# Performance work log

Measured on AMD Instinct MI355X. Metric: run time of the kernel, lower is better.

The kernel has to match this reference:

```python
import jax, jax.numpy as jnp
import numpy as np

EMBED_DIM = 1024
Q_HEADS = 8
KV_HEADS = 4
HEAD_DIM = EMBED_DIM // Q_HEADS          # 128
KV_EMBED_DIM = HEAD_DIM * KV_HEADS       # 512
LN_EPS = 1e-5
RMS_EPS = 1e-6


def _activation_quant(x):
    # per-token int8 quant over last dim
    scale = 127.0 / jnp.clip(jnp.max(jnp.abs(x), axis=-1, keepdims=True), 1e-5)
    return jnp.clip(jnp.round(x * scale), -128, 127) / scale


def _weight_quant(w):
    # ternary (sign) quant with global mean-abs scale
    scale = jnp.mean(jnp.abs(w))
    e = jnp.mean(w)
    return jnp.sign(w - e) * scale


def bit_linear(x, w):
    # fresh RMSNorm with weight=ones (as in the torch code: RMSNorm(d)(x))
    x_norm = x * jax.lax.rsqrt(jnp.mean(x * x, axis=-1, keepdims=True) + RMS_EPS)
    # straight-through estimators
    x_q = x_norm + jax.lax.stop_gradient(_activation_quant(x_norm) - x_norm)
    w_q = w + jax.lax.stop_gradient(_weight_quant(w) - w)
    # F.linear(x_quant, w_quant): NO bias (the torch forward ignores self.bias)
    return jnp.einsum('bnd,od->bno', x_q, w_q)


def setup_inputs() -> dict:
    key = jax.random.key(0)
    ks = jax.random.split(key, 7)
    B, S = 4, 2048

    def xavier(k, shape):
        std = (2.0 / (shape[0] + shape[1])) ** 0.5
        return std * jax.random.normal(k, shape, dtype=jnp.float32)

    return {
        'query': jax.random.normal(ks[0], (B, S, EMBED_DIM), dtype=jnp.float32),
        'key':   jax.random.normal(ks[1], (B, S, EMBED_DIM), dtype=jnp.float32),
        'value': jax.random.normal(ks[2], (B, S, EMBED_DIM), dtype=jnp.float32),
        'q_w':   xavier(ks[3], (EMBED_DIM, EMBED_DIM)),
        'k_w':   xavier(ks[4], (KV_EMBED_DIM, EMBED_DIM)),
        'v_w':   xavier(ks[5], (KV_EMBED_DIM, EMBED_DIM)),
        'out_w': xavier(ks[6], (EMBED_DIM, KV_EMBED_DIM)),
        'ln_gamma': jnp.ones((KV_EMBED_DIM,), dtype=jnp.float32),
        'ln_beta':  jnp.zeros((KV_EMBED_DIM,), dtype=jnp.float32),
    }


def reference(query, key, value, q_w, k_w, v_w, out_w, ln_gamma, ln_beta):
    B, N, _ = query.shape
    q = bit_linear(query, q_w)   # [b, n, embed_dim]
    k = bit_linear(key,   k_w)   # [b, s, kv_embed_dim]
    v = bit_linear(value, v_w)   # [b, s, kv_embed_dim]

    g = Q_HEADS // KV_HEADS  # head groups
    # b n (hq d) -> b hq n d -> b hk g n d  (head index = h*g + g_idx, matching
    # einops 'b (h g) n d -> b g h n d')
    q = q.reshape(B, N, Q_HEADS, HEAD_DIM).transpose(0, 2, 1, 3)
    q = q.reshape(B, KV_HEADS, g, N, HEAD_DIM)
    k = k.reshape(B, -1, KV_HEADS, HEAD_DIM).transpose(0, 2, 1, 3)  # b h s d
    v = v.reshape(B, -1, KV_HEADS, HEAD_DIM).transpose(0, 2, 1, 3)  # b h s d

    scale = HEAD_DIM ** 0.5
    q = q / scale
    # note: the original SUMS over the group axis g (faithful to einops einsum)
    sim = jnp.einsum('bhgnd,bhsd->bhns', q, k)
    # note: original divides by scale AGAIN before softmax
    attn = jax.nn.softmax(sim / scale, axis=-1)
    out = jnp.einsum('bhns,bhsd->bnhd', attn, v)        # b n hk d
    x = out.reshape(B, N, KV_EMBED_DIM)

    # LayerNorm over kv_embed_dim
    mu = jnp.mean(x, axis=-1, keepdims=True)
    var = jnp.mean((x - mu) ** 2, axis=-1, keepdims=True)
    x = (x - mu) * jax.lax.rsqrt(var + LN_EPS) * ln_gamma + ln_beta

    return bit_linear(x, out_w)  # [b, n, embed_dim]
```

## Files before the change

kernel.cpp:

```cpp
#include <hip/hip_runtime.h>
#include <cstdint>
#include <cstddef>

constexpr int B_   = 4;
constexpr int SEQ  = 2048;
constexpr int E    = 1024;
constexpr int KVE  = 512;
constexpr int H    = 4;
constexpr int ROWS = B_ * SEQ;
constexpr int NSPLIT = 2;
constexpr int KVT  = SEQ / NSPLIT;
constexpr int NT   = KVT / 64;

typedef short short8   __attribute__((ext_vector_type(8)));
typedef short short4v  __attribute__((ext_vector_type(4)));
typedef float floatx4  __attribute__((ext_vector_type(4)));
typedef float floatx16 __attribute__((ext_vector_type(16)));
typedef int   intx4    __attribute__((ext_vector_type(4)));

__device__ inline short f2bf(float f) {
    uint32_t u = __builtin_bit_cast(uint32_t, f);
    u = (u + 0x7fff + ((u >> 16) & 1)) >> 16;
    return (short)u;
}
__device__ inline float bf2f(short s) {
    return __builtin_bit_cast(float, (uint32_t)(uint16_t)s << 16);
}
__device__ inline void gl_lds16(const void* g, void* l) {
    __builtin_amdgcn_global_load_lds(
        (const __attribute__((address_space(1))) unsigned int*)g,
        (__attribute__((address_space(3))) unsigned int*)l, 16, 0, 0);
}

__global__ __launch_bounds__(256) void pre_kernel(
    const float* __restrict__ qx, const float* __restrict__ kx,
    const float* __restrict__ vx,
    const float* __restrict__ w0, const float* __restrict__ w1,
    const float* __restrict__ w2, const float* __restrict__ w3,
    int8_t* __restrict__ xq01, int8_t* __restrict__ xq2,
    float* __restrict__ dqv, float* __restrict__ stats)
{
    int tid = threadIdx.x, bid = blockIdx.x;
    int lane = tid & 63, wv = tid >> 6;
    if (bid < 256) {
        int m = bid >> 6;
        const float* w = (m == 0) ? w0 : (m == 1) ? w1 : (m == 2) ? w2 : w3;
        int n4 = ((m == 0) ? 1024 * 1024 : 512 * 1024) >> 2;
        float s = 0.f, sa = 0.f;
        for (int i = (bid & 63) * 256 + tid; i < n4; i += 64 * 256) {
            float4 x = ((const float4*)w)[i];
            s += x.x + x.y + x.z + x.w;
            sa += fabsf(x.x) + fabsf(x.y) + fabsf(x.z) + fabsf(x.w);
        }
#pragma unroll
        for (int o = 32; o; o >>= 1) { s += __shfl_xor(s, o); sa += __shfl_xor(sa, o); }
        __shared__ float ls[4], lsa[4];
        if (!lane) { ls[wv] = s; lsa[wv] = sa; }
        __syncthreads();
        if (!tid) {
            atomicAdd(&stats[2 * m],     ls[0] + ls[1] + ls[2] + ls[3]);
            atomicAdd(&stats[2 * m + 1], lsa[0] + lsa[1] + lsa[2] + lsa[3]);
        }
        return;
    }
    int rowi = (bid - 256) * 4 + wv;
    int z = rowi >> 13, r = rowi & (ROWS - 1);
    const float* x = (z == 0) ? qx : (z == 1) ? kx : vx;
    int8_t* xq = (z == 2) ? xq2 : xq01 + (size_t)z * ROWS * E;
    size_t base = (size_t)r * E;
    float4 v[4];
    float ss = 0.f, am = 0.f;
#pragma unroll
    for (int j = 0; j < 4; j++) {
        v[j] = *(const float4*)(x + base + lane * 4 + j * 256);
        ss += v[j].x * v[j].x + v[j].y * v[j].y + v[j].z * v[j].z + v[j].w * v[j].w;
        am = fmaxf(am, fmaxf(fmaxf(fabsf(v[j].x), fabsf(v[j].y)),
                             fmaxf(fabsf(v[j].z), fabsf(v[j].w))));
    }
#pragma unroll
    for (int o = 32; o; o >>= 1) { ss += __shfl_xor(ss, o); am = fmaxf(am, __shfl_xor(am, o)); }
    float rms = rsqrtf(ss * (1.0f / E) + 1e-6f);
    float cl  = fmaxf(am * rms, 1e-5f);
    float kf  = rms * (127.0f / cl);
#pragma unroll
    for (int j = 0; j < 4; j++) {
        int q0 = max(-128, min(127, (int)rintf(v[j].x * kf)));
        int q1 = max(-128, min(127, (int)rintf(v[j].y * kf)));
        int q2 = max(-128, min(127, (int)rintf(v[j].z * kf)));
        int q3 = max(-128, min(127, (int)rintf(v[j].w * kf)));
        uint32_t pk = (uint32_t)(q0 & 0xff) | ((uint32_t)(q1 & 0xff) << 8) |
                      ((uint32_t)(q2 & 0xff) << 16) | ((uint32_t)(q3 & 0xff) << 24);
        *(uint32_t*)(xq + base + lane * 4 + j * 256) = pk;
    }
    if (!lane) dqv[(size_t)z * ROWS + r] = cl * (1.0f / 127.0f);
}

__global__ __launch_bounds__(256) void wquant_kernel(
    const float* __restrict__ w0, const float* __restrict__ w1,
    const float* __restrict__ w2, const float* __restrict__ w3,
    int n0, int n1, int n2, int n3, const float* __restrict__ stats,
    int8_t* __restrict__ o0, int8_t* __restrict__ o1,
    int8_t* __restrict__ o2, int8_t* __restrict__ o3)
{
    int m = blockIdx.y;
    const float* w = (m == 0) ? w0 : (m == 1) ? w1 : (m == 2) ? w2 : w3;
    int n = (m == 0) ? n0 : (m == 1) ? n1 : (m == 2) ? n2 : n3;
    int8_t* o = (m == 0) ? o0 : (m == 1) ? o1 : (m == 2) ? o2 : o3;
    float e = stats[2 * m] / (float)n;
    int n4 = n >> 2;
    for (int i = blockIdx.x * 256 + threadIdx.x; i < n4; i += gridDim.x * 256) {
        float4 x = ((const float4*)w)[i];
        int q0 = (x.x > e) - (x.x < e);
        int q1 = (x.y > e) - (x.y < e);
        int q2 = (x.z > e) - (x.z < e);
        int q3 = (x.w > e) - (x.w < e);
        uint32_t pk = (uint32_t)(q0 & 0xff) | ((uint32_t)(q1 & 0xff) << 8) |
                      ((uint32_t)(q2 & 0xff) << 16) | ((uint32_t)(q3 & 0xff) << 24);
        *(uint32_t*)(o + ((size_t)i << 2)) = pk;
    }
}

template <bool F32OUT>
__device__ inline void gemm_body(
    const int8_t* __restrict__ A, const int8_t* __restrict__ W,
    const float* __restrict__ dqv, float sw, void* __restrict__ Cout,
    int O, int K, int8_t* As, int8_t* Ws, size_t row0, size_t c0)
{
    int tid = threadIdx.x;
    int w = tid >> 6, lane = tid & 63;
    int quad = lane >> 4, l15 = lane & 15;
    int mbase = (w & 1) * 64, nbase = (w >> 1) * 64;

    intx4 acc[4][4];
#pragma unroll
    for (int i = 0; i < 4; i++)
#pragma unroll
        for (int j = 0; j < 4; j++) acc[i][j] = (intx4){0, 0, 0, 0};

    const int8_t* Ag[4]; const int8_t* Wg[4]; int8_t* lA[4]; int8_t* lW[4];
#pragma unroll
    for (int t = 0; t < 4; t++) {
        int c = tid + t * 256;
        int row = c >> 3, g = (c & 7) ^ (row & 7);
        Ag[t] = A + (row0 + row) * K + g * 16;
        Wg[t] = W + (c0 + row) * K + g * 16;
        lA[t] = As + c * 16;
        lW[t] = Ws + c * 16;
    }

    for (int kt = 0; kt < K; kt += 128) {
        __syncthreads();
#pragma unroll
        for (int t = 0; t < 4; t++) {
            gl_lds16(Ag[t] + kt, lA[t]);
            gl_lds16(Wg[t] + kt, lW[t]);
        }
        __syncthreads();
#pragma unroll
        for (int kh = 0; kh < 2; kh++) {
            intx4 af[4], bfr[4];
#pragma unroll
            for (int mt = 0; mt < 4; mt++) {
                int row = mbase + mt * 16 + l15;
                int pos = (quad + 4 * kh) ^ (row & 7);
                af[mt] = *(const intx4*)(As + row * 128 + pos * 16);
            }
#pragma unroll
            for (int nt = 0; nt < 4; nt++) {
                int row = nbase + nt * 16 + l15;
                int pos = (quad + 4 * kh) ^ (row & 7);
                bfr[nt] = *(const intx4*)(Ws + row * 128 + pos * 16);
            }
#pragma unroll
            for (int mt = 0; mt < 4; mt++)
#pragma unroll
                for (int nt = 0; nt < 4; nt++)
                    acc[mt][nt] = __builtin_amdgcn_mfma_i32_16x16x64_i8(
                        af[mt], bfr[nt], acc[mt][nt], 0, 0, 0);
        }
    }

#pragma unroll
    for (int mt = 0; mt < 4; mt++) {
#pragma unroll
        for (int r = 0; r < 4; r++) {
            size_t grow = row0 + mbase + mt * 16 + quad * 4 + r;
            float scv = sw * dqv[grow];
#pragma unroll
            for (int nt = 0; nt < 4; nt++) {
                size_t gcol = c0 + nbase + nt * 16 + l15;
                float v = (float)acc[mt][nt][r] * scv;
                if constexpr (F32OUT) ((float*)Cout)[grow * O + gcol] = v;
                else                  ((short*)Cout)[grow * O + gcol] = f2bf(v);
            }
        }
    }
}

__global__ __launch_bounds__(256) void gemm_qkv(
    const int8_t* __restrict__ xq01, const int8_t* __restrict__ xq2,
    const int8_t* __restrict__ wq_q, const int8_t* __restrict__ wq_k,
    const int8_t* __restrict__ wq_v, const float* __restrict__ dqv,
    const float* __restrict__ stats,
    short* __restrict__ qb, short* __restrict__ kb, short* __restrict__ vb)
{
    __shared__ int8_t As[128 * 128];
    __shared__ int8_t Ws[128 * 128];
    int id = blockIdx.x;
    int z, bx, by;
    if (id < 512)      { z = 0; bx = id & 7; by = id >> 3; }
    else if (id < 768) { z = 1; int t = id - 512; bx = t & 3; by = t >> 2; }
    else               { z = 2; int t = id - 768; bx = t & 3; by = t >> 2; }
    int O = z ? KVE : E;
    const int8_t* A = (z == 0) ? xq01 : (z == 1) ? xq01 + (size_t)ROWS * E : xq2;
    const int8_t* W = (z == 0) ? wq_q : (z == 1) ? wq_k : wq_v;
    short* outp = (z == 0) ? qb : (z == 1) ? kb : vb;
    float sw = stats[2 * z + 1] / (float)(O * E);
    gemm_body<false>(A, W, dqv + (size_t)z * ROWS, sw, outp, O, E, As, Ws,
                     (size_t)by * 128, (size_t)bx * 128);
}

__global__ __launch_bounds__(256) void gemm_out(
    const int8_t* __restrict__ A, const int8_t* __restrict__ W,
    const float* __restrict__ dqv, const float* __restrict__ stats,
    float* __restrict__ Cout)
{
    __shared__ int8_t As[128 * 128];
    __shared__ int8_t Ws[128 * 128];
    float sw = stats[7] / (float)(E * KVE);
    gemm_body<true>(A, W, dqv, sw, Cout, E, KVE, As, Ws,
                    (size_t)blockIdx.y * 128, (size_t)blockIdx.x * 128);
}

__global__ __launch_bounds__(256, 2) void attn_mfma(
    const short* __restrict__ qb, const short* __restrict__ kb,
    const short* __restrict__ vb, short* __restrict__ opart,
    float* __restrict__ mlbuf)
{
    __shared__ short Ks[64][132];
    __shared__ short Vt[128][68];
    int tid = threadIdx.x;
    int w = tid >> 6, lane = tid & 63;
    int l31 = lane & 31, hi = lane >> 5;
    int blk = blockIdx.x, h = blockIdx.y, part = blockIdx.z;
    int b = blk >> 4;
    size_t qrow0 = (size_t)blk * 128;
    size_t sbase = (size_t)b * SEQ + (size_t)part * KVT;

    int sK = tid >> 2, cK = tid & 3;
    int sV = (tid & 15) * 4, dV = tid >> 4;

    short8 kreg[4], vreg[4];
    {
        const short* ksrc = kb + (sbase + sK) * KVE + h * 128 + cK * 32;
#pragma unroll
        for (int j = 0; j < 4; j++) kreg[j] = *(const short8*)(ksrc + j * 8);
        const short* vsrc = vb + (sbase + sV) * KVE + h * 128 + dV * 8;
#pragma unroll
        for (int j = 0; j < 4; j++) vreg[j] = *(const short8*)(vsrc + j * KVE);
    }

    short8 qfrag[8];
    {
        const short* src = qb + (qrow0 + w * 32 + l31) * E + h * 256 + hi * 8;
        constexpr float C = 1.44269504089f * (1.0f / 128.0f);
#pragma unroll
        for (int j = 0; j < 8; j++) {
            short8 a  = *(const short8*)(src + j * 16);
            short8 b2 = *(const short8*)(src + j * 16 + 128);
            short8 o;
#pragma unroll
            for (int e = 0; e < 8; e++)
                o[e] = f2bf((bf2f(a[e]) + bf2f(b2[e])) * C);
            qfrag[j] = o;
        }
    }

    floatx16 oacc[4];
#pragma unroll
    for (int dt = 0; dt < 4; dt++)
#pragma unroll
        for (int r = 0; r < 16; r++) oacc[dt][r] = 0.f;
    float m_s = -1e30f, l_s = 0.f;

    for (int st = 0; st < NT; st++) {
        __syncthreads();
#pragma unroll
        for (int j = 0; j < 4; j++)
            *(short8*)&Ks[sK][cK * 32 + j * 8] = kreg[j];
#pragma unroll
        for (int i = 0; i < 8; i++) {
            short4v vv = { vreg[0][i], vreg[1][i], vreg[2][i], vreg[3][i] };
            *(short4v*)&Vt[dV * 8 + i][sV] = vv;
        }
        if (st + 1 < NT) {
            size_t srow0 = sbase + (size_t)(st + 1) * 64;
            const short* ksrc = kb + (srow0 + sK) * KVE + h * 128 + cK * 32;
#pragma unroll
            for (int j = 0; j < 4; j++) kreg[j] = *(const short8*)(ksrc + j * 8);
            const short* vsrc = vb + (srow0 + sV) * KVE + h * 128 + dV * 8;
#pragma unroll
            for (int j = 0; j < 4; j++) vreg[j] = *(const short8*)(vsrc + j * KVE);
        }
        __syncthreads();
        floatx16 sc0, sc1;
#pragma unroll
        for (int r = 0; r < 16; r++) { sc0[r] = 0.f; sc1[r] = 0.f; }
#pragma unroll
        for (int j = 0; j < 8; j++) {
            short8 kf0 = *(const short8*)&Ks[l31][j * 16 + hi * 8];
            short8 kf1 = *(const short8*)&Ks[32 + l31][j * 16 + hi * 8];
            sc0 = __builtin_amdgcn_mfma_f32_32x32x16_bf16(kf0, qfrag[j], sc0, 0, 0, 0);
            sc1 = __builtin_amdgcn_mfma_f32_32x32x16_bf16(kf1, qfrag[j], sc1, 0, 0, 0);
        }
        float mx = sc0[0];
#pragma unroll
        for (int r = 0; r < 16; r++) mx = fmaxf(mx, fmaxf(sc0[r], sc1[r]));
        mx = fmaxf(mx, __shfl_xor(mx, 32));
        float pm = fmaxf(m_s, mx);
        if (!__all(pm - m_s <= 8.0f)) {
            float alpha = __builtin_amdgcn_exp2f(m_s - pm);
            m_s = pm;
            l_s *= alpha;
#pragma unroll
            for (int dt = 0; dt < 4; dt++)
#pragma unroll
                for (int r = 0; r < 16; r++) oacc[dt][r] *= alpha;
        }
        float rs = 0.f;
#pragma unroll
        for (int r = 0; r < 16; r++) {
            float p0 = __builtin_amdgcn_exp2f(sc0[r] - m_s); sc0[r] = p0; rs += p0;
            float p1 = __builtin_amdgcn_exp2f(sc1[r] - m_s); sc1[r] = p1; rs += p1;
        }
        rs += __shfl_xor(rs, 32);
        l_s += rs;
        uint32_t w0[8], w1[8];
#pragma unroll
        for (int i = 0; i < 8; i++) {
            asm("v_cvt_pk_bf16_f32 %0, %1, %2"
                : "=v"(w0[i]) : "v"(sc0[2 * i]), "v"(sc0[2 * i + 1]));
            asm("v_cvt_pk_bf16_f32 %0, %1, %2"
                : "=v"(w1[i]) : "v"(sc1[2 * i]), "v"(sc1[2 * i + 1]));
        }
#pragma unroll
        for (int i = 0; i < 2; i++) {
            { auto r = __builtin_amdgcn_permlane32_swap(w0[i], w0[i + 2], false, false);
              w0[i] = r[0]; w0[i + 2] = r[1]; }
            { auto r = __builtin_amdgcn_permlane32_swap(w0[i + 4], w0[i + 6], false, false);
              w0[i + 4] = r[0]; w0[i + 6] = r[1]; }
            { auto r = __builtin_amdgcn_permlane32_swap(w1[i], w1[i + 2], false, false);
              w1[i] = r[0]; w1[i + 2] = r[1]; }
            { auto r = __builtin_amdgcn_permlane32_swap(w1[i + 4], w1[i + 6], false, false);
              w1[i + 4] = r[0]; w1[i + 6] = r[1]; }
        }
        short8 pb[4];
        {
            intx4 t0 = { (int)w0[0], (int)w0[1], (int)w0[2], (int)w0[3] };
            intx4 t1 = { (int)w0[4], (int)w0[5], (int)w0[6], (int)w0[7] };
            intx4 t2 = { (int)w1[0], (int)w1[1], (int)w1[2], (int)w1[3] };
            intx4 t3 = { (int)w1[4], (int)w1[5], (int)w1[6], (int)w1[7] };
            pb[0] = __builtin_bit_cast(short8, t0);
            pb[1] = __builtin_bit_cast(short8, t1);
            pb[2] = __builtin_bit_cast(short8, t2);
            pb[3] = __builtin_bit_cast(short8, t3);
        }
#pragma unroll
        for (int dt = 0; dt < 4; dt++)
#pragma unroll
            for (int j = 0; j < 4; j++) {
                short8 vf = *(const short8*)&Vt[dt * 32 + l31][j * 16 + hi * 8];
                oacc[dt] = __builtin_amdgcn_mfma_f32_32x32x16_bf16(vf, pb[j], oacc[dt], 0, 0, 0);
            }
    }
    {
        float inv = 1.0f / l_s;
        size_t grow = qrow0 + w * 32 + l31;
        short* dst = opart + ((size_t)part * ROWS + grow) * KVE + h * 128;
#pragma unroll
        for (int dt = 0; dt < 4; dt++)
#pragma unroll
            for (int c = 0; c < 4; c++) {
                short4v o4 = { f2bf(oacc[dt][c * 4] * inv),
                               f2bf(oacc[dt][c * 4 + 1] * inv),
                               f2bf(oacc[dt][c * 4 + 2] * inv),
                               f2bf(oacc[dt][c * 4 + 3] * inv) };
                *(short4v*)(dst + dt * 32 + c * 8 + hi * 4) = o4;
            }
        if (hi == 0) {
            float* ml = mlbuf + (((size_t)part * ROWS + grow) * H + h) * 2;
            ml[0] = m_s;
            ml[1] = l_s;
        }
    }
}

__global__ __launch_bounds__(256) void ln_combine_kernel(
    const short* __restrict__ opart, const float* __restrict__ mlbuf,
    const float* __restrict__ gamma, const float* __restrict__ beta,
    int8_t* __restrict__ xq, float* __restrict__ dqv)
{
    int lane = threadIdx.x & 63, wv = threadIdx.x >> 6;
    int row = blockIdx.x * 4 + wv;
    float4 y[2];
    float s = 0.f, ss = 0.f;
#pragma unroll
    for (int j = 0; j < 2; j++) {
        int col = lane * 4 + j * 256;
        int h = j * 2 + (lane >> 5);
        float mv[NSPLIT], lv[NSPLIT];
        float M = -1e30f;
#pragma unroll
        for (int p = 0; p < NSPLIT; p++) {
            const float* ml = mlbuf + (((size_t)p * ROWS + row) * H + h) * 2;
            mv[p] = ml[0]; lv[p] = ml[1];
            M = fmaxf(M, mv[p]);
        }
        float wt[NSPLIT], wsum = 0.f;
#pragma unroll
        for (int p = 0; p < NSPLIT; p++) {
            wt[p] = lv[p] * __builtin_amdgcn_exp2f(mv[p] - M);
            wsum += wt[p];
        }
        float winv = 1.0f / wsum;
        float4 vv = { 0.f, 0.f, 0.f, 0.f };
#pragma unroll
        for (int p = 0; p < NSPLIT; p++) {
            short4v o = *(const short4v*)(opart + ((size_t)p * ROWS + row) * KVE + col);
            float wp = wt[p] * winv;
            vv.x += bf2f(o.x) * wp;
            vv.y += bf2f(o.y) * wp;
            vv.z += bf2f(o.z) * wp;
            vv.w += bf2f(o.w) * wp;
        }
        y[j] = vv;
        s += vv.x + vv.y + vv.z + vv.w;
        ss += vv.x * vv.x + vv.y * vv.y + vv.z * vv.z + vv.w * vv.w;
    }
#pragma unroll
    for (int o = 32; o; o >>= 1) { s += __shfl_xor(s, o); ss += __shfl_xor(ss, o); }
    float mu = s * (1.0f / KVE);
    float var = fmaxf(ss * (1.0f / KVE) - mu * mu, 0.0f);
    float inv = rsqrtf(var + 1e-5f);
    float sy = 0.f, am = 0.f;
#pragma unroll
    for (int j = 0; j < 2; j++) {
        int col = lane * 4 + j * 256;
        float4 g = *(const float4*)(gamma + col);
        float4 be = *(const float4*)(beta + col);
        y[j].x = (y[j].x - mu) * inv * g.x + be.x;
        y[j].y = (y[j].y - mu) * inv * g.y + be.y;
        y[j].z = (y[j].z - mu) * inv * g.z + be.z;
        y[j].w = (y[j].w - mu) * inv * g.w + be.w;
        sy += y[j].x * y[j].x + y[j].y * y[j].y + y[j].z * y[j].z + y[j].w * y[j].w;
        am = fmaxf(am, fmaxf(fmaxf(fabsf(y[j].x), fabsf(y[j].y)),
                             fmaxf(fabsf(y[j].z), fabsf(y[j].w))));
    }
#pragma unroll
    for (int o = 32; o; o >>= 1) { sy += __shfl_xor(sy, o); am = fmaxf(am, __shfl_xor(am, o)); }
    float rms = rsqrtf(sy * (1.0f / KVE) + 1e-6f);
    float cl = fmaxf(am * rms, 1e-5f);
    float kf = rms * (127.0f / cl);
#pragma unroll
    for (int j = 0; j < 2; j++) {
        int col = lane * 4 + j * 256;
        int q0 = max(-128, min(127, (int)rintf(y[j].x * kf)));
        int q1 = max(-128, min(127, (int)rintf(y[j].y * kf)));
        int q2 = max(-128, min(127, (int)rintf(y[j].z * kf)));
        int q3 = max(-128, min(127, (int)rintf(y[j].w * kf)));
        uint32_t pk = (uint32_t)(q0 & 0xff) | ((uint32_t)(q1 & 0xff) << 8) |
                      ((uint32_t)(q2 & 0xff) << 16) | ((uint32_t)(q3 & 0xff) << 24);
        *(uint32_t*)(xq + (size_t)row * KVE + col) = pk;
    }
    if (!lane) dqv[row] = cl * (1.0f / 127.0f);
}

extern "C" void kernel_launch(void* const* d_in, const int* in_sizes, int n_in,
                              void* d_out, int out_size, void* d_ws, size_t ws_size,
                              hipStream_t stream)
{
    const float* query = (const float*)d_in[0];
    const float* key   = (const float*)d_in[1];
    const float* value = (const float*)d_in[2];
    const float* q_w   = (const float*)d_in[3];
    const float* k_w   = (const float*)d_in[4];
    const float* v_w   = (const float*)d_in[5];
    const float* out_w = (const float*)d_in[6];
    const float* ln_g  = (const float*)d_in[7];
    const float* ln_b  = (const float*)d_in[8];
    float* out = (float*)d_out;

    char* p = (char*)d_ws;
    float* stats = (float*)p;  p += 256;
    int8_t* wq_q = (int8_t*)p; p += (size_t)1024 * 1024;
    int8_t* wq_k = (int8_t*)p; p += (size_t)512 * 1024;
    int8_t* wq_v = (int8_t*)p; p += (size_t)512 * 1024;
    int8_t* wq_o = (int8_t*)p; p += (size_t)1024 * 512;
    int8_t* xq01 = (int8_t*)p; p += (size_t)2 * ROWS * E;
    float* dqv  = (float*)p;   p += (size_t)3 * ROWS * 4;
    short* qb   = (short*)p;   p += (size_t)ROWS * E * 2;
    short* kb   = (short*)p;   p += (size_t)ROWS * KVE * 2;
    short* vb   = (short*)p;   p += (size_t)ROWS * KVE * 2;
    short* opart = (short*)p;  p += (size_t)NSPLIT * ROWS * KVE * 2;
    float* mlbuf = (float*)p;  p += (size_t)NSPLIT * ROWS * H * 2 * 4;
    int8_t* xq2 = (int8_t*)opart;
    if ((size_t)(p - (char*)d_ws) > ws_size) return;

    dim3 blk(256);
    hipMemsetAsync(stats, 0, 256, stream);
    pre_kernel<<<dim3(256 + 3 * ROWS / 4), blk, 0, stream>>>(query, key, value,
        q_w, k_w, v_w, out_w, xq01, xq2, dqv, stats);
    wquant_kernel<<<dim3(64, 4), blk, 0, stream>>>(q_w, k_w, v_w, out_w,
        1024 * 1024, 512 * 1024, 512 * 1024, 1024 * 512, stats, wq_q, wq_k, wq_v, wq_o);

    gemm_qkv<<<dim3(1024), blk, 0, stream>>>(xq01, xq2, wq_q, wq_k, wq_v,
        dqv, stats, qb, kb, vb);

    attn_mfma<<<dim3(ROWS / 128, H, NSPLIT), blk, 0, stream>>>(qb, kb, vb,
        opart, mlbuf);

    ln_combine_kernel<<<dim3(ROWS / 4), blk, 0, stream>>>(opart, mlbuf,
        ln_g, ln_b, xq01, dqv);
    gemm_out<<<dim3(8, 64), blk, 0, stream>>>(xq01, wq_o, dqv, stats, out);
}
```

Before: 261.5 us.

## Split attention KV tile across wave pairs with in-block softmax merge

Each attention block now handles 64 query rows instead of 128. The four waves form a 2x2 grid: two query groups and two KV halves of every 64-key tile. Each wave computes only a 32x32 score tile, and the two KV-half partials are merged at the end through shared memory using their running max and sum. This halves the per-wave accumulator and score registers, allowing 4 blocks per CU and a doubled grid for more occupancy. The cost is that K/V tiles are reloaded by twice as many blocks, plus extra shared-memory traffic and syncs for the final merge.

```diff
diff --git a/kernel.cpp b/kernel.cpp
--- a/kernel.cpp
+++ b/kernel.cpp
@@ -232,19 +232,24 @@
                     (size_t)blockIdx.y * 128, (size_t)blockIdx.x * 128);
 }
 
-__global__ __launch_bounds__(256, 2) void attn_mfma(
+__global__ __launch_bounds__(256, 4) void attn_mfma(
     const short* __restrict__ qb, const short* __restrict__ kb,
     const short* __restrict__ vb, short* __restrict__ opart,
     float* __restrict__ mlbuf)
 {
-    __shared__ short Ks[64][132];
-    __shared__ short Vt[128][68];
+    __shared__ __align__(16) char smem[34816];
+    short (*Ks)[132] = (short (*)[132])smem;
+    short (*Vt)[68]  = (short (*)[68])(smem + 16896);
+    float (*Om)[133] = (float (*)[133])smem;
+    float* mlw       = (float*)(smem + 34048);
+
     int tid = threadIdx.x;
     int w = tid >> 6, lane = tid & 63;
     int l31 = lane & 31, hi = lane >> 5;
+    int qg = w & 1, kg = w >> 1;
     int blk = blockIdx.x, h = blockIdx.y, part = blockIdx.z;
-    int b = blk >> 4;
-    size_t qrow0 = (size_t)blk * 128;
+    int b = blk >> 5;
+    size_t qrow0 = (size_t)blk * 64;
     size_t sbase = (size_t)b * SEQ + (size_t)part * KVT;
 
     int sK = tid >> 2, cK = tid & 3;
@@ -262,7 +267,7 @@
 
     short8 qfrag[8];
     {
-        const short* src = qb + (qrow0 + w * 32 + l31) * E + h * 256 + hi * 8;
+        const short* src = qb + (qrow0 + qg * 32 + l31) * E + h * 256 + hi * 8;
         constexpr float C = 1.44269504089f * (1.0f / 128.0f);
 #pragma unroll
         for (int j = 0; j < 8; j++) {
@@ -303,19 +308,17 @@
             for (int j = 0; j < 4; j++) vreg[j] = *(const short8*)(vsrc + j * KVE);
         }
         __syncthreads();
-        floatx16 sc0, sc1;
-#pragma unroll
-        for (int r = 0; r < 16; r++) { sc0[r] = 0.f; sc1[r] = 0.f; }
+        floatx16 sc;
+#pragma unroll
+        for (int r = 0; r < 16; r++) sc[r] = 0.f;
 #pragma unroll
         for (int j = 0; j < 8; j++) {
-            short8 kf0 = *(const short8*)&Ks[l31][j * 16 + hi * 8];
-            short8 kf1 = *(const short8*)&Ks[32 + l31][j * 16 + hi * 8];
-            sc0 = __builtin_amdgcn_mfma_f32_32x32x16_bf16(kf0, qfrag[j], sc0, 0, 0, 0);
-            sc1 = __builtin_amdgcn_mfma_f32_32x32x16_bf16(kf1, qfrag[j], sc1, 0, 0, 0);
-        }
-        float mx = sc0[0];
-#pragma unroll
-        for (int r = 0; r < 16; r++) mx = fmaxf(mx, fmaxf(sc0[r], sc1[r]));
+            short8 kf = *(const short8*)&Ks[kg * 32 + l31][j * 16 + hi * 8];
+            sc = __builtin_amdgcn_mfma_f32_32x32x16_bf16(kf, qfrag[j], sc, 0, 0, 0);
+        }
+        float mx = sc[0];
+#pragma unroll
+        for (int r = 1; r < 16; r++) mx = fmaxf(mx, sc[r]);
         mx = fmaxf(mx, __shfl_xor(mx, 32));
         float pm = fmaxf(m_s, mx);
         if (!__all(pm - m_s <= 8.0f)) {
@@ -330,18 +333,15 @@
         float rs = 0.f;
 #pragma unroll
         for (int r = 0; r < 16; r++) {
-            float p0 = __builtin_amdgcn_exp2f(sc0[r] - m_s); sc0[r] = p0; rs += p0;
-            float p1 = __builtin_amdgcn_exp2f(sc1[r] - m_s); sc1[r] = p1; rs += p1;
+            float p0 = __builtin_amdgcn_exp2f(sc[r] - m_s); sc[r] = p0; rs += p0;
         }
         rs += __shfl_xor(rs, 32);
         l_s += rs;
-        uint32_t w0[8], w1[8];
+        uint32_t w0[8];
 #pragma unroll
         for (int i = 0; i < 8; i++) {
             asm("v_cvt_pk_bf16_f32 %0, %1, %2"
-                : "=v"(w0[i]) : "v"(sc0[2 * i]), "v"(sc0[2 * i + 1]));
-            asm("v_cvt_pk_bf16_f32 %0, %1, %2"
-                : "=v"(w1[i]) : "v"(sc1[2 * i]), "v"(sc1[2 * i + 1]));
+                : "=v"(w0[i]) : "v"(sc[2 * i]), "v"(sc[2 * i + 1]));
         }
 #pragma unroll
         for (int i = 0; i < 2; i++) {
@@ -349,48 +349,65 @@
               w0[i] = r[0]; w0[i + 2] = r[1]; }
             { auto r = __builtin_amdgcn_permlane32_swap(w0[i + 4], w0[i + 6], false, false);
               w0[i + 4] = r[0]; w0[i + 6] = r[1]; }
-            { auto r = __builtin_amdgcn_permlane32_swap(w1[i], w1[i + 2], false, false);
-              w1[i] = r[0]; w1[i + 2] = r[1]; }
-            { auto r = __builtin_amdgcn_permlane32_swap(w1[i + 4], w1[i + 6], false, false);
-              w1[i + 4] = r[0]; w1[i + 6] = r[1]; }
-        }
-        short8 pb[4];
+        }
+        short8 pb[2];
         {
             intx4 t0 = { (int)w0[0], (int)w0[1], (int)w0[2], (int)w0[3] };
             intx4 t1 = { (int)w0[4], (int)w0[5], (int)w0[6], (int)w0[7] };
-            intx4 t2 = { (int)w1[0], (int)w1[1], (int)w1[2], (int)w1[3] };
-            intx4 t3 = { (int)w1[4], (int)w1[5], (int)w1[6], (int)w1[7] };
             pb[0] = __builtin_bit_cast(short8, t0);
             pb[1] = __builtin_bit_cast(short8, t1);
-            pb[2] = __builtin_bit_cast(short8, t2);
-            pb[3] = __builtin_bit_cast(short8, t3);
         }
 #pragma unroll
         for (int dt = 0; dt < 4; dt++)
 #pragma unroll
-            for (int j = 0; j < 4; j++) {
-                short8 vf = *(const short8*)&Vt[dt * 32 + l31][j * 16 + hi * 8];
+            for (int j = 0; j < 2; j++) {
+                short8 vf = *(const short8*)&Vt[dt * 32 + l31][kg * 32 + j * 16 + hi * 8];
                 oacc[dt] = __builtin_amdgcn_mfma_f32_32x32x16_bf16(vf, pb[j], oacc[dt], 0, 0, 0);
             }
     }
-    {
-        float inv = 1.0f / l_s;
-        size_t grow = qrow0 + w * 32 + l31;
+    __syncthreads();
+    if (kg == 1) {
+#pragma unroll
+        for (int dt = 0; dt < 4; dt++)
+#pragma unroll
+            for (int r = 0; r < 16; r++) {
+                int d = dt * 32 + ((r >> 2) << 3) + hi * 4 + (r & 3);
+                Om[qg * 32 + l31][d] = oacc[dt][r];
+            }
+        if (hi == 0) {
+            mlw[qg * 64 + l31 * 2]     = m_s;
+            mlw[qg * 64 + l31 * 2 + 1] = l_s;
+        }
+    }
+    __syncthreads();
+    if (kg == 0) {
+        float m1 = mlw[qg * 64 + l31 * 2];
+        float l1 = mlw[qg * 64 + l31 * 2 + 1];
+        float M  = fmaxf(m_s, m1);
+        float a0 = __builtin_amdgcn_exp2f(m_s - M);
+        float a1 = __builtin_amdgcn_exp2f(m1 - M);
+        float lm = l_s * a0 + l1 * a1;
+        float linv = 1.0f / lm;
+        float s0 = a0 * linv, s1 = a1 * linv;
+        size_t grow = qrow0 + qg * 32 + l31;
         short* dst = opart + ((size_t)part * ROWS + grow) * KVE + h * 128;
+        const float* om = Om[qg * 32 + l31];
 #pragma unroll
         for (int dt = 0; dt < 4; dt++)
 #pragma unroll
             for (int c = 0; c < 4; c++) {
-                short4v o4 = { f2bf(oacc[dt][c * 4] * inv),
-                               f2bf(oacc[dt][c * 4 + 1] * inv),
-                               f2bf(oacc[dt][c * 4 + 2] * inv),
-                               f2bf(oacc[dt][c * 4 + 3] * inv) };
-                *(short4v*)(dst + dt * 32 + c * 8 + hi * 4) = o4;
+                int d = dt * 32 + c * 8 + hi * 4;
+                short4v o4 = {
+                    f2bf(oacc[dt][c * 4 + 0] * s0 + om[d + 0] * s1),
+                    f2bf(oacc[dt][c * 4 + 1] * s0 + om[d + 1] * s1),
+                    f2bf(oacc[dt][c * 4 + 2] * s0 + om[d + 2] * s1),
+                    f2bf(oacc[dt][c * 4 + 3] * s0 + om[d + 3] * s1) };
+                *(short4v*)(dst + d) = o4;
             }
         if (hi == 0) {
             float* ml = mlbuf + (((size_t)part * ROWS + grow) * H + h) * 2;
-            ml[0] = m_s;
-            ml[1] = l_s;
+            ml[0] = M;
+            ml[1] = lm;
         }
     }
 }
@@ -516,7 +533,7 @@
     gemm_qkv<<<dim3(1024), blk, 0, stream>>>(xq01, xq2, wq_q, wq_k, wq_v,
         dqv, stats, qb, kb, vb);
 
-    attn_mfma<<<dim3(ROWS / 128, H, NSPLIT), blk, 0, stream>>>(qb, kb, vb,
+    attn_mfma<<<dim3(ROWS / 64, H, NSPLIT), blk, 0, stream>>>(qb, kb, vb,
         opart, mlbuf);
 
     ln_combine_kernel<<<dim3(ROWS / 4), blk, 0, stream>>>(opart, mlbuf,
```

New measurement: 409.0 us. 56.4% more time.
